# Kernel optimization log

Measured on AMD Instinct MI355X. Metric: run time of the kernel, lower is better.

## Reference

```python
import jax, jax.numpy as jnp
import numpy as np

R, K, D = 4096, 128, 128      # num_records, num_codes, code_dim
B, P = 8, 8192                # batch_size, num_points
DIST_SCALE = 2.0
IN_DIM = D + 3                # 131


def setup_inputs() -> dict:
    key = jax.random.key(0)
    ks = jax.random.split(key, 20)
    inp = {}
    inp["indices"] = jax.random.randint(ks[0], (B,), 0, R)
    inp["query_points"] = jax.random.uniform(ks[1], (B, P, 3)) - 0.5
    inp["codes_position"] = jax.random.uniform(ks[2], (R, K, 3)) - 0.5
    inp["codes"] = jax.random.normal(ks[3], (R, K, D)) * 0.01
    dims = [(IN_DIM, 2048), (IN_DIM + 2048, 1024), (IN_DIM + 1024, 512),
            (IN_DIM + 512, 256), (IN_DIM + 256, 128), (128, 1)]
    for i, (fi, fo) in enumerate(dims):
        inp[f"W{i+1}"] = jax.random.normal(ks[4 + 2 * i], (fi, fo)) * (1.0 / np.sqrt(fi))
        inp[f"b{i+1}"] = jnp.zeros((fo,), jnp.float32)
    return inp


def _lrelu(x):
    return jnp.where(x > 0, x, 0.02 * x)


def reference(indices, query_points, codes_position, codes,
              W1, b1, W2, b2, W3, b3, W4, b4, W5, b5, W6, b6):
    # CodeCloud.query
    bcp = codes_position[indices]                      # (B,K,3)
    bc = codes[indices]                                # (B,K,D)
    diff = query_points[:, :, None, :] - bcp[:, None, :, :]   # (B,P,K,3)
    square_dist = jnp.sum(diff * diff, axis=-1) + 1e-16       # (B,P,K)
    # 1/sqrt(sd)**s == sd**(-s/2)
    weight = square_dist ** (-DIST_SCALE / 2.0)
    weight = weight / jnp.sum(weight, axis=-1, keepdims=True)
    query_codes = jnp.einsum('bpk,bkd->bpd', weight, bc)      # (B,P,D)

    # IM_Decoder with skip concats
    x = jnp.concatenate([query_codes, query_points], axis=-1) # (B,P,IN_DIM)
    h = _lrelu(x @ W1 + b1); h = jnp.concatenate([h, x], axis=-1)
    h = _lrelu(h @ W2 + b2); h = jnp.concatenate([h, x], axis=-1)
    h = _lrelu(h @ W3 + b3); h = jnp.concatenate([h, x], axis=-1)
    h = _lrelu(h @ W4 + b4); h = jnp.concatenate([h, x], axis=-1)
    h = _lrelu(h @ W5 + b5)
    pred_sd = (h @ W6 + b6)[..., 0]                            # (B,P)
    return pred_sd
```

## Files before the change

### kernel.cpp

```cpp
#include <hip/hip_runtime.h>
#include <cstdint>
#include <cstddef>

typedef unsigned short u16;
typedef __attribute__((ext_vector_type(8))) short short8;
typedef __attribute__((ext_vector_type(8))) unsigned short us8;
typedef __attribute__((ext_vector_type(4))) unsigned short us4;
typedef __attribute__((ext_vector_type(4))) float f32x4;
typedef __attribute__((ext_vector_type(2))) unsigned u32x2;

#define BATCH 8
#define PTS   8192
#define NPTS  (BATCH * PTS)
#define KC    128
#define DC    128

__device__ __forceinline__ float bf2f(u16 h) {
  union { unsigned u; float f; } v; v.u = ((unsigned)h) << 16; return v.f;
}
__device__ __forceinline__ u16 f2bf(float f) {
  union { float f; unsigned u; } v; v.f = f;
  unsigned r = v.u + 0x7FFFu + ((v.u >> 16) & 1u);
  return (u16)(r >> 16);
}

__device__ __forceinline__ bool detect_f32(const u16* p, int lane) {
  float v = bf2f(p[2 * lane]);
  float av = v < 0.f ? -v : v;
  return __ballot(av > 4.0f) != 0ULL;
}

__device__ __forceinline__ float ldf(const void* p, size_t i, bool f32) {
  return f32 ? ((const float*)p)[i] : bf2f(((const u16*)p)[i]);
}

__device__ __forceinline__ void gload16(const void* g, void* l) {
  __builtin_amdgcn_global_load_lds(
      (const __attribute__((address_space(1))) unsigned int*)(uintptr_t)g,
      (__attribute__((address_space(3))) unsigned int*)(uintptr_t)l,
      16, 0, 0);
}

__global__ __launch_bounds__(256)
void transpose_w(const void* __restrict__ W, u16* __restrict__ Wt,
                 int fi, int fo, int kp) {
  const bool f32 = detect_f32((const u16*)W, threadIdx.x & 63);
  __shared__ __align__(16) u16 tile[32][33];
  const int k0 = blockIdx.x * 32;
  const int n0 = blockIdx.y * 32;
  const int tx = threadIdx.x & 31;
  const int ty = threadIdx.x >> 5;
  #pragma unroll
  for (int i = 0; i < 4; ++i) {
    int k = k0 + ty + 8 * i;
    u16 v = 0;
    if (k < fi) {
      size_t idx = (size_t)k * fo + (n0 + tx);
      v = f32 ? f2bf(((const float*)W)[idx]) : ((const u16*)W)[idx];
    }
    tile[ty + 8 * i][tx] = v;
  }
  __syncthreads();
  #pragma unroll
  for (int i = 0; i < 4; ++i) {
    int n = n0 + ty + 8 * i;
    Wt[(size_t)n * kp + (k0 + tx)] = tile[tx][ty + 8 * i];
  }
}

__global__ __launch_bounds__(256)
void interp_kernel(const int* __restrict__ indices,
                   const void* __restrict__ qp,
                   const void* __restrict__ cp,
                   const void* __restrict__ codes,
                   u16* __restrict__ d0, int ld0,
                   u16* __restrict__ d1, int ld1,
                   u16* __restrict__ d2, int ld2,
                   u16* __restrict__ d3, int ld3,
                   u16* __restrict__ d4, int ld4,
                   int m0) {
  __shared__ __align__(16) u16 s_bc[KC * DC];
  __shared__ float s_cp[KC * 3];
  __shared__ float s_qp[32 * 3];
  __shared__ float s_w[32 * 132];
  __shared__ float s_part[32 * 4];
  __shared__ float s_winv[32];

  const int t = threadIdx.x;
  const bool f32 = detect_f32((const u16*)codes, t & 63);
  const int row0 = blockIdx.x * 32;
  const int gp0 = m0 + row0;
  const int b = gp0 / PTS;
  const int rec = indices[b];

  if (f32) {
    const float* src = (const float*)codes + (size_t)rec * (KC * DC);
    #pragma unroll
    for (int i = 0; i < 16; ++i) {
      int off = (t + i * 256) * 4;
      float4 v = *(const float4*)&src[off];
      us4 o; o.x = f2bf(v.x); o.y = f2bf(v.y); o.z = f2bf(v.z); o.w = f2bf(v.w);
      *(us4*)&s_bc[off] = o;
    }
  } else {
    const u16* src = (const u16*)codes + (size_t)rec * (KC * DC);
    #pragma unroll
    for (int i = 0; i < 8; ++i) {
      int off = (t + i * 256) * 8;
      *(us8*)&s_bc[off] = *(const us8*)&src[off];
    }
  }
  if (t < KC) {
    size_t base = ((size_t)rec * KC + t) * 3;
    s_cp[t * 3 + 0] = ldf(cp, base + 0, f32);
    s_cp[t * 3 + 1] = ldf(cp, base + 1, f32);
    s_cp[t * 3 + 2] = ldf(cp, base + 2, f32);
  }
  if (t < 96) {
    int i = t / 3, c = t - i * 3;
    s_qp[t] = ldf(qp, (size_t)(gp0 + i) * 3 + c, f32);
  }
  __syncthreads();

  #pragma unroll
  for (int it = 0; it < 16; ++it) {
    int idx = t + it * 256;
    int k = idx & 127, p = idx >> 7;
    float dx = s_qp[p * 3 + 0] - s_cp[k * 3 + 0];
    float dy = s_qp[p * 3 + 1] - s_cp[k * 3 + 1];
    float dz = s_qp[p * 3 + 2] - s_cp[k * 3 + 2];
    float dsq = dx * dx + dy * dy + dz * dz + 1e-16f;
    s_w[p * 132 + k] = 1.0f / dsq;
  }
  __syncthreads();
  if (t < 128) {
    int p = t >> 2, part = t & 3;
    float s = 0.f;
    #pragma unroll
    for (int j = 0; j < 32; ++j) s += s_w[p * 132 + part * 32 + j];
    s_part[p * 4 + part] = s;
  }
  __syncthreads();
  if (t < 32) {
    float s = s_part[t * 4 + 0] + s_part[t * 4 + 1] + s_part[t * 4 + 2] + s_part[t * 4 + 3];
    s_winv[t] = 1.0f / s;
  }
  __syncthreads();

  {
    int p = t >> 3;
    int dd = (t & 7) * 16;
    float acc[16];
    #pragma unroll
    for (int j = 0; j < 16; ++j) acc[j] = 0.f;
    for (int k = 0; k < KC; ++k) {
      float wv = s_w[p * 132 + k];
      us8 v0 = *(const us8*)&s_bc[k * DC + dd];
      us8 v1 = *(const us8*)&s_bc[k * DC + dd + 8];
      #pragma unroll
      for (int j = 0; j < 8; ++j) acc[j] += wv * bf2f(v0[j]);
      #pragma unroll
      for (int j = 0; j < 8; ++j) acc[8 + j] += wv * bf2f(v1[j]);
    }
    float wi = s_winv[p];
    us8 o0, o1;
    #pragma unroll
    for (int j = 0; j < 8; ++j) { o0[j] = f2bf(acc[j] * wi); o1[j] = f2bf(acc[8 + j] * wi); }
    size_t row = (size_t)(row0 + p);
    *(us8*)&d0[row * ld0 + dd] = o0; *(us8*)&d0[row * ld0 + dd + 8] = o1;
    *(us8*)&d1[row * ld1 + dd] = o0; *(us8*)&d1[row * ld1 + dd + 8] = o1;
    *(us8*)&d2[row * ld2 + dd] = o0; *(us8*)&d2[row * ld2 + dd + 8] = o1;
    *(us8*)&d3[row * ld3 + dd] = o0; *(us8*)&d3[row * ld3 + dd + 8] = o1;
    *(us8*)&d4[row * ld4 + dd] = o0; *(us8*)&d4[row * ld4 + dd + 8] = o1;
  }

  if (t < 32) {
    size_t row = (size_t)(row0 + t);
    us8 z = {0, 0, 0, 0, 0, 0, 0, 0};
    us8 t0 = z;
    t0[0] = f2bf(s_qp[t * 3 + 0]);
    t0[1] = f2bf(s_qp[t * 3 + 1]);
    t0[2] = f2bf(s_qp[t * 3 + 2]);
    u16* ps[5] = {d0, d1, d2, d3, d4};
    int  ls[5] = {ld0, ld1, ld2, ld3, ld4};
    #pragma unroll
    for (int qd = 0; qd < 5; ++qd) {
      u16* dst = ps[qd] + row * ls[qd] + 128;
      *(us8*)&dst[0] = t0;
      #pragma unroll
      for (int c = 1; c < 8; ++c) *(us8*)&dst[c * 8] = z;
    }
  }
}

__global__ __launch_bounds__(256, 2)
void gemm_bt_lrelu(const u16* __restrict__ A, int lda,
                   const u16* __restrict__ Bt, int ldb,
                   const u16* __restrict__ bias,
                   u16* __restrict__ C, int ldc,
                   int Kp) {
  __shared__ __align__(16) u16 sA[128 * 32];
  __shared__ __align__(16) u16 sB[128 * 32];
  const int tid = threadIdx.x;
  const int lane = tid & 63;
  const int w = tid >> 6;
  const int wm = w & 1, wn = w >> 1;
  const int bn = blockIdx.x * 128, bm = blockIdx.y * 128;

  const f32x4 zero = {0.f, 0.f, 0.f, 0.f};
  f32x4 acc[4][4];
  #pragma unroll
  for (int i = 0; i < 4; ++i)
    #pragma unroll
    for (int j = 0; j < 4; ++j) acc[i][j] = zero;

  const int r4 = lane >> 2;
  const int cg = lane & 3;
  const u16* ag = A + (size_t)(bm + w * 32 + r4) * lda + cg * 8;
  const u16* bg = Bt + (size_t)(bn + w * 32 + r4) * ldb + cg * 8;
  u16* la = &sA[w * 1024];
  u16* lb = &sB[w * 1024];

  const int r = lane & 15, q = lane >> 4;
  const u16* ra = &sA[(wm * 64 + r) * 32 + q * 8];
  const u16* rb = &sB[(wn * 64 + r) * 32 + q * 8];

  for (int k0 = 0; k0 < Kp; k0 += 32) {
    gload16(ag + k0, la);
    gload16(ag + k0 + (size_t)16 * lda, la + 512);
    gload16(bg + k0, lb);
    gload16(bg + k0 + (size_t)16 * ldb, lb + 512);
    __syncthreads();
    short8 af[4], bq[4];
    #pragma unroll
    for (int mt = 0; mt < 4; ++mt) af[mt] = *(const short8*)(ra + mt * 512);
    #pragma unroll
    for (int nt = 0; nt < 4; ++nt) bq[nt] = *(const short8*)(rb + nt * 512);
    #pragma unroll
    for (int mt = 0; mt < 4; ++mt)
      #pragma unroll
      for (int nt = 0; nt < 4; ++nt)
        acc[mt][nt] = __builtin_amdgcn_mfma_f32_16x16x32_bf16(af[mt], bq[nt], acc[mt][nt], 0, 0, 0);
    __syncthreads();
  }

  #pragma unroll
  for (int nt = 0; nt < 4; ++nt) {
    int col = bn + wn * 64 + nt * 16 + r;
    float bb = bf2f(bias[col]);
    #pragma unroll
    for (int mt = 0; mt < 4; ++mt) {
      int grow = bm + wm * 64 + mt * 16 + q * 4;
      #pragma unroll
      for (int reg = 0; reg < 4; ++reg) {
        float v = acc[mt][nt][reg] + bb;
        v = v > 0.f ? v : 0.02f * v;
        C[(size_t)(grow + reg) * ldc + col] = f2bf(v);
      }
    }
  }
}

#define G_BAR()  __builtin_amdgcn_s_barrier()
#define G_FENCE() asm volatile("" ::: "memory")
#define G_LGKM0() asm volatile("s_waitcnt lgkmcnt(0)" ::: "memory")

__global__ __launch_bounds__(512, 2)
void gemm256_bt_lrelu(const u16* __restrict__ A, int lda,
                      const u16* __restrict__ Bt, int ldb,
                      const u16* __restrict__ bias,
                      u16* __restrict__ C, int ldc,
                      int Kp, int lognx) {
  __shared__ __align__(16) u16 smem[65536 + 256];
  u16* sA = smem;
  u16* sB = smem + 32768;
  u16* sbias = smem + 65536;

  const int tid = threadIdx.x;
  const int lane = tid & 63;
  const int w = tid >> 6;
  const int wm = w >> 2;
  const int wn = w & 3;
  const int lr = lane & 15;
  const int kg = lane >> 4;
  const int rs = tid >> 3;
  const int cs = ((tid & 7) ^ (rs & 7)) << 3;

  const unsigned nwg = gridDim.x;
  const unsigned lid = blockIdx.x;
  const unsigned qq = nwg >> 3, rr = nwg & 7, xc = lid & 7, ii = lid >> 3;
  const unsigned swz = (xc < rr ? xc * (qq + 1) : rr * (qq + 1) + (xc - rr) * qq) + ii;
  const int bx = (int)(swz & ((1u << lognx) - 1u));
  const int by = (int)(swz >> lognx);
  const int bn = bx << 8, bm = by << 8;

  const u16* a0 = A + (size_t)(bm + rs) * lda + cs;
  const u16* b0 = Bt + (size_t)(bn + rs) * ldb + cs;

  if (tid < 64) *(us4*)&sbias[tid << 2] = *(const us4*)&bias[bn + (tid << 2)];

  const int rowA = (wm << 13) + (lr << 6);
  const int rowB = (wn << 12) + (lr << 6);
  const int c0 = ((kg ^ (lr & 7)) << 3);
  const int c1 = (((4 + kg) ^ (lr & 7)) << 3);

  const int nt = Kp >> 6;

  f32x4 acc[8][4];
  const f32x4 zero = {0.f, 0.f, 0.f, 0.f};
  #pragma unroll
  for (int m = 0; m < 8; ++m)
    #pragma unroll
    for (int n = 0; n < 4; ++n) acc[m][n] = zero;

#define STAGE_A(bfv, h, kt) do { \
    const u16* _s = a0 + (size_t)(h) * 128 * lda + ((kt) << 6); \
    u16* _d = &sA[((bfv) << 14) + ((h) << 13) + (tid << 3)]; \
    gload16(_s, _d); \
    gload16(_s + (size_t)64 * lda, _d + 4096); \
  } while (0)
#define STAGE_B(bfv, h, kt) do { \
    const u16* _s = b0 + (size_t)(h) * 128 * ldb + ((kt) << 6); \
    u16* _d = &sB[((bfv) << 14) + ((h) << 13) + (tid << 3)]; \
    gload16(_s, _d); \
    gload16(_s + (size_t)64 * ldb, _d + 4096); \
  } while (0)

  STAGE_B(0, 0, 0); STAGE_B(0, 1, 0); STAGE_A(0, 0, 0); STAGE_A(0, 1, 0);
  if (nt > 1) {
    STAGE_B(1, 0, 1); STAGE_B(1, 1, 1); STAGE_A(1, 0, 1);
    asm volatile("s_waitcnt vmcnt(6)" ::: "memory");
  } else {
    asm volatile("s_waitcnt vmcnt(0)" ::: "memory");
  }
  G_BAR(); G_FENCE();

  short8 af[4][2], bq[4][2];

  for (int t = 0; t < nt; ++t) {
    const int sb = (t & 1) << 14;
    #pragma unroll
    for (int m = 0; m < 4; ++m) {
      af[m][0] = *(const short8*)&sA[sb + rowA + (m << 10) + c0];
      af[m][1] = *(const short8*)&sA[sb + rowA + (m << 10) + c1];
    }
    #pragma unroll
    for (int n = 0; n < 4; ++n) {
      bq[n][0] = *(const short8*)&sB[sb + rowB + (n << 10) + c0];
      bq[n][1] = *(const short8*)&sB[sb + rowB + (n << 10) + c1];
    }
    if (t + 1 < nt) STAGE_A((t & 1) ^ 1, 1, t + 1);
    G_FENCE(); G_BAR(); G_FENCE();
    __builtin_amdgcn_s_setprio(1);
    #pragma unroll
    for (int k = 0; k < 2; ++k)
      #pragma unroll
      for (int m = 0; m < 4; ++m)
        #pragma unroll
        for (int n = 0; n < 2; ++n)
          acc[m][n] = __builtin_amdgcn_mfma_f32_16x16x32_bf16(bq[n][k], af[m][k], acc[m][n], 0, 0, 0);
    __builtin_amdgcn_s_setprio(0);
    G_LGKM0();
    G_BAR(); G_FENCE();
    if (t + 2 < nt) STAGE_B(t & 1, 0, t + 2);
    G_FENCE(); G_BAR(); G_FENCE();
    __builtin_amdgcn_s_setprio(1);
    #pragma unroll
    for (int k = 0; k < 2; ++k)
      #pragma unroll
      for (int m = 0; m < 4; ++m)
        #pragma unroll
        for (int n = 0; n < 2; ++n)
          acc[m][n + 2] = __builtin_amdgcn_mfma_f32_16x16x32_bf16(bq[n + 2][k], af[m][k], acc[m][n + 2], 0, 0, 0);
    __builtin_amdgcn_s_setprio(0);
    G_BAR(); G_FENCE();
    #pragma unroll
    for (int m = 0; m < 4; ++m) {
      af[m][0] = *(const short8*)&sA[sb + rowA + ((m + 4) << 10) + c0];
      af[m][1] = *(const short8*)&sA[sb + rowA + ((m + 4) << 10) + c1];
    }
    if (t + 2 < nt) STAGE_B(t & 1, 1, t + 2);
    G_FENCE(); G_BAR(); G_FENCE();
    __builtin_amdgcn_s_setprio(1);
    #pragma unroll
    for (int k = 0; k < 2; ++k)
      #pragma unroll
      for (int m = 0; m < 4; ++m)
        #pragma unroll
        for (int n = 0; n < 2; ++n)
          acc[m + 4][n] = __builtin_amdgcn_mfma_f32_16x16x32_bf16(bq[n][k], af[m][k], acc[m + 4][n], 0, 0, 0);
    __builtin_amdgcn_s_setprio(0);
    G_LGKM0();
    G_BAR(); G_FENCE();
    if (t + 2 < nt) STAGE_A(t & 1, 0, t + 2);
    G_FENCE(); G_BAR(); G_FENCE();
    __builtin_amdgcn_s_setprio(1);
    #pragma unroll
    for (int k = 0; k < 2; ++k)
      #pragma unroll
      for (int m = 0; m < 4; ++m)
        #pragma unroll
        for (int n = 0; n < 2; ++n)
          acc[m + 4][n + 2] = __builtin_amdgcn_mfma_f32_16x16x32_bf16(bq[n + 2][k], af[m][k], acc[m + 4][n + 2], 0, 0, 0);
    __builtin_amdgcn_s_setprio(0);
    if (t + 2 < nt)      { asm volatile("s_waitcnt vmcnt(6)" ::: "memory"); }
    else if (t + 1 < nt) { asm volatile("s_waitcnt vmcnt(0)" ::: "memory"); }
    G_BAR(); G_FENCE();
  }
#undef STAGE_A
#undef STAGE_B

  u16* sC = smem;
  const int colq = (wn << 6) + (kg << 2);
  float bias_v[4][4];
  #pragma unroll
  for (int n = 0; n < 4; ++n) {
    us4 bb = *(const us4*)&sbias[colq + (n << 4)];
    #pragma unroll
    for (int j = 0; j < 4; ++j) bias_v[n][j] = bf2f(bb[j]);
  }
  #pragma unroll
  for (int pass = 0; pass < 2; ++pass) {
    if (wm == pass) {
      #pragma unroll
      for (int m = 0; m < 8; ++m) {
        const int row = (m << 4) + lr;
        #pragma unroll
        for (int n = 0; n < 4; ++n) {
          f32x4 a = acc[m][n];
          float v0 = a[0] + bias_v[n][0]; v0 = v0 > 0.f ? v0 : 0.02f * v0;
          float v1 = a[1] + bias_v[n][1]; v1 = v1 > 0.f ? v1 : 0.02f * v1;
          float v2 = a[2] + bias_v[n][2]; v2 = v2 > 0.f ? v2 : 0.02f * v2;
          float v3 = a[3] + bias_v[n][3]; v3 = v3 > 0.f ? v3 : 0.02f * v3;
          u32x2 d;
          d.x = (unsigned)f2bf(v0) | ((unsigned)f2bf(v1) << 16);
          d.y = (unsigned)f2bf(v2) | ((unsigned)f2bf(v3) << 16);
          *(u32x2*)&sC[row * 264 + colq + (n << 4)] = d;
        }
      }
      G_LGKM0();
    }
    G_BAR();
    {
      const int rrow = tid >> 5;
      const int cc = (tid & 31) << 3;
      #pragma unroll
      for (int it = 0; it < 8; ++it) {
        const int row = (it << 4) + rrow;
        us8 v = *(const us8*)&sC[row * 264 + cc];
        *(us8*)&C[(size_t)(bm + (pass << 7) + row) * ldc + bn + cc] = v;
      }
    }
    G_BAR();
  }
}

__global__ __launch_bounds__(256)
void final_dot(const u16* __restrict__ h5, const void* __restrict__ W6,
               const u16* __restrict__ b6, void* __restrict__ out, int m0) {
  __shared__ float s_w6[128];
  const int t = threadIdx.x;
  const bool f32 = detect_f32((const u16*)W6, t & 63);
  if (t < 128) s_w6[t] = ldf(W6, t, f32);
  __syncthreads();
  const size_t row = (size_t)blockIdx.x * 256 + t;
  const u16* hp = h5 + row * 128;
  float acc = 0.f;
  #pragma unroll
  for (int i = 0; i < 16; ++i) {
    us8 v = *(const us8*)&hp[i * 8];
    #pragma unroll
    for (int j = 0; j < 8; ++j) acc += bf2f(v[j]) * s_w6[i * 8 + j];
  }
  acc += bf2f(b6[0]);
  if (f32) ((float*)out)[m0 + row] = acc;
  else     ((u16*)out)[m0 + row] = f2bf(acc);
}

extern "C" void kernel_launch(void* const* d_in, const int* in_sizes, int n_in,
                              void* d_out, int out_size, void* d_ws, size_t ws_size,
                              hipStream_t stream) {
  (void)in_sizes; (void)n_in; (void)out_size;
  const int* indices = (const int*)d_in[0];
  const void* qp    = d_in[1];
  const void* cp    = d_in[2];
  const void* codes = d_in[3];
  const void* Wm[6]; const u16* bv[6];
  for (int i = 0; i < 6; ++i) { Wm[i] = d_in[4 + 2 * i]; bv[i] = (const u16*)d_in[5 + 2 * i]; }

  static const int fi[5] = {131, 2179, 1155, 643, 387};
  static const int fo[5] = {2048, 1024, 512, 256, 128};
  static const int kp[5] = {192, 2240, 1216, 704, 448};
  static const int bw[6] = {192, 2240, 1216, 704, 448, 128};

  char* base = (char*)d_ws;
  size_t off = 0;
  u16* wt[5];
  for (int l = 0; l < 5; ++l) {
    wt[l] = (u16*)(base + off);
    off = (off + (size_t)kp[l] * fo[l] * 2 + 255) & ~(size_t)255;
  }
  const size_t fixed = off;

  int CH = 128;
  for (int c = 1; c <= 128; c <<= 1) {
    size_t mc = (size_t)NPTS / c;
    size_t need = fixed;
    for (int i = 0; i < 6; ++i) need += ((mc * bw[i] * 2 + 255) & ~(size_t)255);
    if (need <= ws_size) { CH = c; break; }
  }
  const size_t Mc = (size_t)NPTS / CH;
  u16* ab[6];
  for (int i = 0; i < 6; ++i) {
    ab[i] = (u16*)(base + off);
    off = (off + Mc * bw[i] * 2 + 255) & ~(size_t)255;
  }

  for (int l = 0; l < 5; ++l) {
    dim3 g(kp[l] / 32, fo[l] / 32);
    hipLaunchKernelGGL(transpose_w, g, dim3(256), 0, stream, Wm[l], wt[l], fi[l], fo[l], kp[l]);
  }

  const int nM256 = (int)(Mc >> 8);
  const int nM128 = (int)(Mc >> 7);
  for (int c = 0; c < CH; ++c) {
    int m0 = (int)((size_t)c * Mc);
    hipLaunchKernelGGL(interp_kernel, dim3((unsigned)(Mc / 32)), dim3(256), 0, stream,
                       indices, qp, cp, codes,
                       ab[0], 192,
                       ab[1] + 2048, 2240,
                       ab[2] + 1024, 1216,
                       ab[3] + 512, 704,
                       ab[4] + 256, 448,
                       m0);
    hipLaunchKernelGGL(gemm256_bt_lrelu, dim3((unsigned)(8 * nM256)), dim3(512), 0, stream,
                       ab[0], 192,  wt[0], 192,  bv[0], ab[1], 2240, 192,  3);
    hipLaunchKernelGGL(gemm256_bt_lrelu, dim3((unsigned)(4 * nM256)), dim3(512), 0, stream,
                       ab[1], 2240, wt[1], 2240, bv[1], ab[2], 1216, 2240, 2);
    hipLaunchKernelGGL(gemm256_bt_lrelu, dim3((unsigned)(2 * nM256)), dim3(512), 0, stream,
                       ab[2], 1216, wt[2], 1216, bv[2], ab[3], 704,  1216, 1);
    hipLaunchKernelGGL(gemm256_bt_lrelu, dim3((unsigned)(1 * nM256)), dim3(512), 0, stream,
                       ab[3], 704,  wt[3], 704,  bv[3], ab[4], 448,  704,  0);
    hipLaunchKernelGGL(gemm_bt_lrelu, dim3(1, (unsigned)nM128), dim3(256), 0, stream,
                       ab[4], 448,  wt[4], 448,  bv[4], ab[5], 128,  448);
    hipLaunchKernelGGL(final_dot, dim3((unsigned)(Mc / 256)), dim3(256), 0, stream,
                       ab[5], Wm[5], bv[5], (void*)d_out, m0);
  }
}
```

Baseline: 921.5 us.

## Read skip input from shared buffer and fuse final dot into last GEMM

The interpolation kernel now writes the concatenated input x once into a single 192-wide buffer instead of copying it into five per-layer activation buffers. The GEMM kernels switch their A-operand source from the layer activation to that shared x buffer once past a K split point, so each activation buffer only holds the layer output. The last GEMM folds in bias, leaky ReLU and the 128-to-1 dot with W6 through shuffle reductions and shared memory, which removes the separate final_dot kernel and the h5 round trip. This adds a per-K-step branch in the load path and more epilogue work in the fused kernel.

```diff
diff --git a/kernel.cpp b/kernel.cpp
--- a/kernel.cpp
+++ b/kernel.cpp
@@ -14,6 +14,7 @@
 #define NPTS  (BATCH * PTS)
 #define KC    128
 #define DC    128
+#define XW    192
 
 __device__ __forceinline__ float bf2f(u16 h) {
   union { unsigned u; float f; } v; v.u = ((unsigned)h) << 16; return v.f;
@@ -73,11 +74,7 @@
                    const void* __restrict__ qp,
                    const void* __restrict__ cp,
                    const void* __restrict__ codes,
-                   u16* __restrict__ d0, int ld0,
-                   u16* __restrict__ d1, int ld1,
-                   u16* __restrict__ d2, int ld2,
-                   u16* __restrict__ d3, int ld3,
-                   u16* __restrict__ d4, int ld4,
+                   u16* __restrict__ xb,
                    int m0) {
   __shared__ __align__(16) u16 s_bc[KC * DC];
   __shared__ float s_cp[KC * 3];
@@ -167,11 +164,8 @@
     #pragma unroll
     for (int j = 0; j < 8; ++j) { o0[j] = f2bf(acc[j] * wi); o1[j] = f2bf(acc[8 + j] * wi); }
     size_t row = (size_t)(row0 + p);
-    *(us8*)&d0[row * ld0 + dd] = o0; *(us8*)&d0[row * ld0 + dd + 8] = o1;
-    *(us8*)&d1[row * ld1 + dd] = o0; *(us8*)&d1[row * ld1 + dd + 8] = o1;
-    *(us8*)&d2[row * ld2 + dd] = o0; *(us8*)&d2[row * ld2 + dd + 8] = o1;
-    *(us8*)&d3[row * ld3 + dd] = o0; *(us8*)&d3[row * ld3 + dd + 8] = o1;
-    *(us8*)&d4[row * ld4 + dd] = o0; *(us8*)&d4[row * ld4 + dd + 8] = o1;
+    *(us8*)&xb[row * XW + dd] = o0;
+    *(us8*)&xb[row * XW + dd + 8] = o1;
   }
 
   if (t < 32) {
@@ -181,31 +175,32 @@
     t0[0] = f2bf(s_qp[t * 3 + 0]);
     t0[1] = f2bf(s_qp[t * 3 + 1]);
     t0[2] = f2bf(s_qp[t * 3 + 2]);
-    u16* ps[5] = {d0, d1, d2, d3, d4};
-    int  ls[5] = {ld0, ld1, ld2, ld3, ld4};
-    #pragma unroll
-    for (int qd = 0; qd < 5; ++qd) {
-      u16* dst = ps[qd] + row * ls[qd] + 128;
-      *(us8*)&dst[0] = t0;
-      #pragma unroll
-      for (int c = 1; c < 8; ++c) *(us8*)&dst[c * 8] = z;
-    }
+    u16* dst = xb + row * XW + 128;
+    *(us8*)&dst[0] = t0;
+    *(us8*)&dst[8] = z;
+    *(us8*)&dst[16] = z;
+    *(us8*)&dst[24] = z;
   }
 }
 
 __global__ __launch_bounds__(256, 2)
-void gemm_bt_lrelu(const u16* __restrict__ A, int lda,
+void gemm_fused_l5(const u16* __restrict__ A, int lda,
+                   const u16* __restrict__ X,
+                   int splitE,
                    const u16* __restrict__ Bt, int ldb,
-                   const u16* __restrict__ bias,
-                   u16* __restrict__ C, int ldc,
-                   int Kp) {
+                   const u16* __restrict__ b5,
+                   const void* __restrict__ W6,
+                   const u16* __restrict__ b6,
+                   void* __restrict__ out, int m0, int Kp) {
   __shared__ __align__(16) u16 sA[128 * 32];
   __shared__ __align__(16) u16 sB[128 * 32];
+  __shared__ float s_red[128][2];
   const int tid = threadIdx.x;
   const int lane = tid & 63;
   const int w = tid >> 6;
   const int wm = w & 1, wn = w >> 1;
-  const int bn = blockIdx.x * 128, bm = blockIdx.y * 128;
+  const int bm = blockIdx.y * 128;
+  const bool f32o = detect_f32((const u16*)W6, lane);
 
   const f32x4 zero = {0.f, 0.f, 0.f, 0.f};
   f32x4 acc[4][4];
@@ -217,7 +212,8 @@
   const int r4 = lane >> 2;
   const int cg = lane & 3;
   const u16* ag = A + (size_t)(bm + w * 32 + r4) * lda + cg * 8;
-  const u16* bg = Bt + (size_t)(bn + w * 32 + r4) * ldb + cg * 8;
+  const u16* xg = X + (size_t)(bm + w * 32 + r4) * XW + cg * 8;
+  const u16* bg = Bt + (size_t)(w * 32 + r4) * ldb + cg * 8;
   u16* la = &sA[w * 1024];
   u16* lb = &sB[w * 1024];
 
@@ -226,8 +222,14 @@
   const u16* rb = &sB[(wn * 64 + r) * 32 + q * 8];
 
   for (int k0 = 0; k0 < Kp; k0 += 32) {
-    gload16(ag + k0, la);
-    gload16(ag + k0 + (size_t)16 * lda, la + 512);
+    if (k0 < splitE) {
+      gload16(ag + k0, la);
+      gload16(ag + k0 + (size_t)16 * lda, la + 512);
+    } else {
+      const u16* xs = xg + (k0 - splitE);
+      gload16(xs, la);
+      gload16(xs + (size_t)16 * XW, la + 512);
+    }
     gload16(bg + k0, lb);
     gload16(bg + k0 + (size_t)16 * ldb, lb + 512);
     __syncthreads();
@@ -244,20 +246,48 @@
     __syncthreads();
   }
 
+  float w6v[4], b5v[4];
   #pragma unroll
   for (int nt = 0; nt < 4; ++nt) {
-    int col = bn + wn * 64 + nt * 16 + r;
-    float bb = bf2f(bias[col]);
-    #pragma unroll
-    for (int mt = 0; mt < 4; ++mt) {
-      int grow = bm + wm * 64 + mt * 16 + q * 4;
+    int col = wn * 64 + nt * 16 + r;
+    w6v[nt] = ldf(W6, col, f32o);
+    b5v[nt] = bf2f(b5[col]);
+  }
+  float part[4][4];
+  #pragma unroll
+  for (int mt = 0; mt < 4; ++mt)
+    #pragma unroll
+    for (int reg = 0; reg < 4; ++reg) part[mt][reg] = 0.f;
+  #pragma unroll
+  for (int nt = 0; nt < 4; ++nt)
+    #pragma unroll
+    for (int mt = 0; mt < 4; ++mt)
       #pragma unroll
       for (int reg = 0; reg < 4; ++reg) {
-        float v = acc[mt][nt][reg] + bb;
+        float v = acc[mt][nt][reg] + b5v[nt];
         v = v > 0.f ? v : 0.02f * v;
-        C[(size_t)(grow + reg) * ldc + col] = f2bf(v);
+        part[mt][reg] += v * w6v[nt];
       }
-    }
+  #pragma unroll
+  for (int off = 1; off < 16; off <<= 1)
+    #pragma unroll
+    for (int mt = 0; mt < 4; ++mt)
+      #pragma unroll
+      for (int reg = 0; reg < 4; ++reg)
+        part[mt][reg] += __shfl_xor(part[mt][reg], off, 64);
+  if (r == 0) {
+    #pragma unroll
+    for (int mt = 0; mt < 4; ++mt)
+      #pragma unroll
+      for (int reg = 0; reg < 4; ++reg)
+        s_red[wm * 64 + mt * 16 + q * 4 + reg][wn] = part[mt][reg];
+  }
+  __syncthreads();
+  if (tid < 128) {
+    float s = s_red[tid][0] + s_red[tid][1] + bf2f(b6[0]);
+    size_t grow = (size_t)m0 + bm + tid;
+    if (f32o) ((float*)out)[grow] = s;
+    else      ((u16*)out)[grow] = f2bf(s);
   }
 }
 
@@ -267,6 +297,7 @@
 
 __global__ __launch_bounds__(512, 2)
 void gemm256_bt_lrelu(const u16* __restrict__ A, int lda,
+                      const u16* __restrict__ X, int ksplit,
                       const u16* __restrict__ Bt, int ldb,
                       const u16* __restrict__ bias,
                       u16* __restrict__ C, int ldc,
@@ -295,6 +326,7 @@
   const int bn = bx << 8, bm = by << 8;
 
   const u16* a0 = A + (size_t)(bm + rs) * lda + cs;
+  const u16* x0 = X + (size_t)(bm + rs) * XW + cs;
   const u16* b0 = Bt + (size_t)(bn + rs) * ldb + cs;
 
   if (tid < 64) *(us4*)&sbias[tid << 2] = *(const us4*)&bias[bn + (tid << 2)];
@@ -314,13 +346,15 @@
     for (int n = 0; n < 4; ++n) acc[m][n] = zero;
 
 #define STAGE_A(bfv, h, kt) do { \
-    const u16* _s = a0 + (size_t)(h) * 128 * lda + ((kt) << 6); \
+    const u16* _s; size_t _st; \
+    if ((kt) < ksplit) { _s = a0 + (size_t)(h) * 128 * lda + ((size_t)(kt) << 6); _st = (size_t)64 * lda; } \
+    else               { _s = x0 + (size_t)(h) * 128 * XW + ((size_t)((kt) - ksplit) << 6); _st = (size_t)64 * XW; } \
     u16* _d = &sA[((bfv) << 14) + ((h) << 13) + (tid << 3)]; \
     gload16(_s, _d); \
-    gload16(_s + (size_t)64 * lda, _d + 4096); \
+    gload16(_s + _st, _d + 4096); \
   } while (0)
 #define STAGE_B(bfv, h, kt) do { \
-    const u16* _s = b0 + (size_t)(h) * 128 * ldb + ((kt) << 6); \
+    const u16* _s = b0 + (size_t)(h) * 128 * ldb + ((size_t)(kt) << 6); \
     u16* _d = &sB[((bfv) << 14) + ((h) << 13) + (tid << 3)]; \
     gload16(_s, _d); \
     gload16(_s + (size_t)64 * ldb, _d + 4096); \
@@ -455,28 +489,6 @@
   }
 }
 
-__global__ __launch_bounds__(256)
-void final_dot(const u16* __restrict__ h5, const void* __restrict__ W6,
-               const u16* __restrict__ b6, void* __restrict__ out, int m0) {
-  __shared__ float s_w6[128];
-  const int t = threadIdx.x;
-  const bool f32 = detect_f32((const u16*)W6, t & 63);
-  if (t < 128) s_w6[t] = ldf(W6, t, f32);
-  __syncthreads();
-  const size_t row = (size_t)blockIdx.x * 256 + t;
-  const u16* hp = h5 + row * 128;
-  float acc = 0.f;
-  #pragma unroll
-  for (int i = 0; i < 16; ++i) {
-    us8 v = *(const us8*)&hp[i * 8];
-    #pragma unroll
-    for (int j = 0; j < 8; ++j) acc += bf2f(v[j]) * s_w6[i * 8 + j];
-  }
-  acc += bf2f(b6[0]);
-  if (f32) ((float*)out)[m0 + row] = acc;
-  else     ((u16*)out)[m0 + row] = f2bf(acc);
-}
-
 extern "C" void kernel_launch(void* const* d_in, const int* in_sizes, int n_in,
                               void* d_out, int out_size, void* d_ws, size_t ws_size,
                               hipStream_t stream) {
@@ -491,7 +503,7 @@
   static const int fi[5] = {131, 2179, 1155, 643, 387};
   static const int fo[5] = {2048, 1024, 512, 256, 128};
   static const int kp[5] = {192, 2240, 1216, 704, 448};
-  static const int bw[6] = {192, 2240, 1216, 704, 448, 128};
+  static const int bw[5] = {192, 2048, 1024, 512, 256};
 
   char* base = (char*)d_ws;
   size_t off = 0;
@@ -506,12 +518,12 @@
   for (int c = 1; c <= 128; c <<= 1) {
     size_t mc = (size_t)NPTS / c;
     size_t need = fixed;
-    for (int i = 0; i < 6; ++i) need += ((mc * bw[i] * 2 + 255) & ~(size_t)255);
+    for (int i = 0; i < 5; ++i) need += ((mc * bw[i] * 2 + 255) & ~(size_t)255);
     if (need <= ws_size) { CH = c; break; }
   }
   const size_t Mc = (size_t)NPTS / CH;
-  u16* ab[6];
-  for (int i = 0; i < 6; ++i) {
+  u16* ab[5];
+  for (int i = 0; i < 5; ++i) {
     ab[i] = (u16*)(base + off);
     off = (off + Mc * bw[i] * 2 + 255) & ~(size_t)255;
   }
@@ -526,24 +538,17 @@
   for (int c = 0; c < CH; ++c) {
     int m0 = (int)((size_t)c * Mc);
     hipLaunchKernelGGL(interp_kernel, dim3((unsigned)(Mc / 32)), dim3(256), 0, stream,
-                       indices, qp, cp, codes,
-                       ab[0], 192,
-                       ab[1] + 2048, 2240,
-                       ab[2] + 1024, 1216,
-                       ab[3] + 512, 704,
-                       ab[4] + 256, 448,
-                       m0);
+                       indices, qp, cp, codes, ab[0], m0);
     hipLaunchKernelGGL(gemm256_bt_lrelu, dim3((unsigned)(8 * nM256)), dim3(512), 0, stream,
-                       ab[0], 192,  wt[0], 192,  bv[0], ab[1], 2240, 192,  3);
+                       ab[0], 192,  ab[0], 64, wt[0], 192,  bv[0], ab[1], 2048, 192,  3);
     hipLaunchKernelGGL(gemm256_bt_lrelu, dim3((unsigned)(4 * nM256)), dim3(512), 0, stream,
-                       ab[1], 2240, wt[1], 2240, bv[1], ab[2], 1216, 2240, 2);
+                       ab[1], 2048, ab[0], 32, wt[1], 2240, bv[1], ab[2], 1024, 2240, 2);
     hipLaunchKernelGGL(gemm256_bt_lrelu, dim3((unsigned)(2 * nM256)), dim3(512), 0, stream,
-                       ab[2], 1216, wt[2], 1216, bv[2], ab[3], 704,  1216, 1);
+                       ab[2], 1024, ab[0], 16, wt[2], 1216, bv[2], ab[3], 512,  1216, 1);
     hipLaunchKernelGGL(gemm256_bt_lrelu, dim3((unsigned)(1 * nM256)), dim3(512), 0, stream,
-                       ab[3], 704,  wt[3], 704,  bv[3], ab[4], 448,  704,  0);
-    hipLaunchKernelGGL(gemm_bt_lrelu, dim3(1, (unsigned)nM128), dim3(256), 0, stream,
-                       ab[4], 448,  wt[4], 448,  bv[4], ab[5], 128,  448);
-    hipLaunchKernelGGL(final_dot, dim3((unsigned)(Mc / 256)), dim3(256), 0, stream,
-                       ab[5], Wm[5], bv[5], (void*)d_out, m0);
-  }
-}
+                       ab[3], 512,  ab[0], 8,  wt[3], 704,  bv[3], ab[4], 256,  704,  0);
+    hipLaunchKernelGGL(gemm_fused_l5, dim3(1, (unsigned)nM128), dim3(256), 0, stream,
+                       ab[4], 256, ab[0], 256, wt[4], 448, bv[4], Wm[5], bv[5],
+                       (void*)d_out, m0, 448);
+  }
+}
```

New measurement: 917.5 us. No clear change (-0.4%).
